# Optimization experiments

Measured on AMD Instinct MI355X. Metric: run time of the kernel, lower is better.

Reference implementation:

```python
import jax, jax.numpy as jnp
import numpy as np

B, S, E = 2, 2048, 1024
HID = 1024
HEADS = 16
EPS = 1e-5
SCALE = (E * 2) ** (-0.5)  # source uses input_data_dim*2


def setup_inputs() -> dict:
    key = jax.random.key(0)
    k1, k2, k3 = jax.random.split(key, 3)
    return {
        "x": jax.random.normal(k1, (B, S, E), dtype=jnp.float32),
        "ln_g": jnp.ones((E,), jnp.float32),
        "ln_b": jnp.zeros((E,), jnp.float32),
        "W1": jax.random.normal(k2, (E, 3 * HID), jnp.float32) * 0.02,
        "b1": jnp.zeros((3 * HID,), jnp.float32),
        "W2": jax.random.normal(k3, (HID, HID), jnp.float32) * 0.02,
        "b2": jnp.zeros((HID,), jnp.float32),
    }


def reference(x, ln_g, ln_b, W1, b1, W2, b2):
    # LayerNorm over last dim
    mu = jnp.mean(x, axis=-1, keepdims=True)
    var = jnp.mean(jnp.square(x - mu), axis=-1, keepdims=True)
    xn = (x - mu) * jax.lax.rsqrt(var + EPS) * ln_g + ln_b
    # QKV projection: [B,S,3*HID]
    qkv = jnp.einsum('bse,ef->bsf', xn, W1) + b1
    # Faithful to source: flat reshape to (heads, B, S, 3*HID/heads)
    qkv_heads = qkv.reshape(HEADS, B, S, -1)
    q, k, v = jnp.split(qkv_heads, 3, axis=-1)  # each [H,B,S,d]
    scores = jnp.einsum('hbse,hbSe->hbsS', q, k) * SCALE  # [H,B,S,S]
    att = jax.nn.softmax(scores, axis=-1)
    full_att = jnp.einsum('hbsS,hbSe->hbse', att, v)  # [H,B,S,d]
    full_att = full_att.reshape(B, S, -1)  # faithful flat reshape -> [B,S,HID]
    out = jnp.einsum('bsh,hk->bsk', full_att, W2) + b2
    return out
```

## Files before the change

### kernel.cpp

```cpp
#include <hip/hip_runtime.h>

typedef unsigned short u16;
typedef __bf16 bf16x8 __attribute__((ext_vector_type(8)));
typedef float f32x4 __attribute__((ext_vector_type(4)));

static constexpr float SCALE2 = 0.022097086912079608f * 1.4426950408889634f;

__device__ __forceinline__ u16 f2b(float f) {
  union { float f; unsigned int i; } v; v.f = f;
  unsigned int r = v.i + 0x7fffu + ((v.i >> 16) & 1u);
  return (u16)(r >> 16);
}
__device__ __forceinline__ unsigned int pk2(float a, float b) {
#if __has_builtin(__builtin_amdgcn_cvt_pk_bf16_f32)
  auto v = __builtin_amdgcn_cvt_pk_bf16_f32(a, b);
  unsigned int u;
  __builtin_memcpy(&u, &v, 4);
  return u;
#else
  union { float f; unsigned int i; } x, y; x.f = a; y.f = b;
  return ((x.i + 0x8000u) >> 16) | ((y.i + 0x8000u) & 0xffff0000u);
#endif
}
__device__ __forceinline__ void async16(const u16* g, u16* l) {
  __builtin_amdgcn_global_load_lds((const __attribute__((address_space(1))) void*)g,
                                   (__attribute__((address_space(3))) void*)l,
                                   16, 0, 0);
}

__global__ __launch_bounds__(256) void pre_kernel(const float* __restrict__ x,
                                                  const float* __restrict__ lg,
                                                  const float* __restrict__ lb,
                                                  u16* __restrict__ xn,
                                                  const float* __restrict__ W1,
                                                  u16* __restrict__ W1T,
                                                  const float* __restrict__ W2,
                                                  u16* __restrict__ W2T) {
  __shared__ __align__(16) u16 smem[64 * 72];
  const int bx = blockIdx.x;
  const int t = threadIdx.x;
  if (bx < 4096) {
    float* red = (float*)smem;
    const int row = bx;
    float4 v = *(const float4*)(x + (size_t)row * 1024 + t * 4);
    float s = v.x + v.y + v.z + v.w;
    float ss = v.x * v.x + v.y * v.y + v.z * v.z + v.w * v.w;
    for (int off = 32; off >= 1; off >>= 1) {
      s += __shfl_xor(s, off, 64);
      ss += __shfl_xor(ss, off, 64);
    }
    const int w = t >> 6;
    if ((t & 63) == 0) { red[w] = s; red[4 + w] = ss; }
    __syncthreads();
    s = red[0] + red[1] + red[2] + red[3];
    ss = red[4] + red[5] + red[6] + red[7];
    const float mu = s * (1.0f / 1024.0f);
    const float var = ss * (1.0f / 1024.0f) - mu * mu;
    const float inv = rsqrtf(var + 1e-5f);
    float4 gg = *(const float4*)(lg + t * 4);
    float4 bb = *(const float4*)(lb + t * 4);
    ushort4 o;
    o.x = f2b((v.x - mu) * inv * gg.x + bb.x);
    o.y = f2b((v.y - mu) * inv * gg.y + bb.y);
    o.z = f2b((v.z - mu) * inv * gg.z + bb.z);
    o.w = f2b((v.w - mu) * inv * gg.w + bb.w);
    *(ushort4*)(xn + (size_t)row * 1024 + t * 4) = o;
    return;
  }
  const float* in;
  u16* out;
  int C, c0, r0;
  if (bx < 4096 + 768) {
    const int idx = bx - 4096;
    C = 3072; in = W1; out = W1T;
    c0 = (idx % 48) * 64; r0 = (idx / 48) * 64;
  } else {
    const int idx = bx - 4864;
    C = 1024; in = W2; out = W2T;
    c0 = (idx % 16) * 64; r0 = (idx / 16) * 64;
  }
  const int row = t >> 2, cseg = t & 3;
  for (int it = 0; it < 4; it++) {
    float4 v = *(const float4*)&in[(size_t)(r0 + row) * C + c0 + it * 16 + cseg * 4];
    ushort4 o;
    o.x = f2b(v.x); o.y = f2b(v.y); o.z = f2b(v.z); o.w = f2b(v.w);
    *(ushort4*)&smem[row * 72 + it * 16 + cseg * 4] = o;
  }
  __syncthreads();
  const int orow = t >> 2, ch = t & 3;
  u16 vals[16];
  for (int j = 0; j < 16; j++) vals[j] = smem[(ch * 16 + j) * 72 + orow];
  u16* dp = out + (size_t)(c0 + orow) * 1024 + r0 + ch * 16;
  *(uint4*)&dp[0] = *(uint4*)&vals[0];
  *(uint4*)&dp[8] = *(uint4*)&vals[8];
}

template <int MODE, int MT>
__global__ __launch_bounds__(256) void gemm_bt(const u16* __restrict__ A,
                                               const u16* __restrict__ Bt,
                                               const float* __restrict__ bias,
                                               float* __restrict__ C,
                                               int M, int N, int K,
                                               u16* __restrict__ Qc,
                                               u16* __restrict__ Kc,
                                               u16* __restrict__ Vtmp) {
  __shared__ __align__(16) u16 SMEM[8192];
  u16* As = SMEM;
  u16* Bs = SMEM + MT * 32;
  const int m0 = blockIdx.y * MT, n0 = blockIdx.x * 128;
  const int t = threadIdx.x, w = t >> 6, lane = t & 63;
  const int q = lane >> 4, l16 = lane & 15;
  const int wm = (w >> 1) * (MT / 2), wn = (w & 1) * 64;
  constexpr int NI = MT / 32;

  const int sc = (lane & 3) ^ ((lane >> 3) & 3);
  const u16* ap = A + (size_t)(m0 + w * 16 + (lane >> 2)) * K + sc * 8;
  const u16* bp = Bt + (size_t)(n0 + w * 16 + (lane >> 2)) * K + sc * 8;
  u16* lA = &As[w * 512];
  u16* lB = &Bs[w * 512];
  const int ac = q ^ ((l16 >> 1) & 3);

  f32x4 acc[NI][4];
  const f32x4 zero = {0.f, 0.f, 0.f, 0.f};
  for (int i = 0; i < NI; i++)
    for (int j = 0; j < 4; j++) acc[i][j] = zero;

  for (int k0 = 0; k0 < K; k0 += 32) {
    for (int i = 0; i < MT / 64; i++)
      async16(ap + (size_t)(i * 64) * K, lA + i * 2048);
    for (int i = 0; i < 2; i++)
      async16(bp + (size_t)(i * 64) * K, lB + i * 2048);
    ap += 32; bp += 32;
    __syncthreads();
    bf16x8 af[NI], bfr[4];
    for (int i = 0; i < NI; i++)
      af[i] = *(const bf16x8*)&As[(wm + i * 16 + l16) * 32 + ac * 8];
    for (int j = 0; j < 4; j++)
      bfr[j] = *(const bf16x8*)&Bs[(wn + j * 16 + l16) * 32 + ac * 8];
    for (int i = 0; i < NI; i++)
      for (int j = 0; j < 4; j++)
        acc[i][j] = __builtin_amdgcn_mfma_f32_16x16x32_bf16(af[i], bfr[j], acc[i][j], 0, 0, 0);
    __syncthreads();
  }

  if constexpr (MODE == 0) {
    for (int j = 0; j < 4; j++) {
      const int col = n0 + wn + j * 16 + l16;
      const float bv = bias[col];
      for (int i = 0; i < NI; i++) {
        const int rbase = m0 + wm + i * 16 + q * 4;
        for (int r = 0; r < 4; r++)
          C[(size_t)(rbase + r) * N + col] = acc[i][j][r] + bv;
      }
    }
  } else {
    const int seg = n0 + wn;
    const int k64 = seg >> 6;
    const int tcol = k64 / 3;
    const int typ = k64 - tcol * 3;
    u16* dst = (typ == 0) ? Qc : (typ == 1) ? Kc : Vtmp;
    const float qs = (typ == 0) ? SCALE2 : 1.0f;
    const int gidx = m0 >> 7;
    u16* tw = &SMEM[w * 1280];
    float bv[4];
    for (int j = 0; j < 4; j++) bv[j] = bias[seg + j * 16 + l16];
    __syncthreads();
    for (int i = 0; i < 4; i++) {
      for (int j = 0; j < 4; j++) {
        ushort4 pk;
        pk.x = f2b((acc[i][j][0] + bv[j]) * qs);
        pk.y = f2b((acc[i][j][1] + bv[j]) * qs);
        pk.z = f2b((acc[i][j][2] + bv[j]) * qs);
        pk.w = f2b((acc[i][j][3] + bv[j]) * qs);
        *(ushort4*)&tw[(j * 16 + l16) * 20 + q * 4] = pk;
      }
      const int r2 = lane >> 2;
      const int quarter = lane & 3;
      u16 vals[16];
      for (int c = 0; c < 16; c++)
        vals[c] = tw[(quarter * 16 + c) * 20 + r2];
      const int lr = wm + i * 16 + r2;
      const int s = (lr << 4) + tcol;
      u16* dp = dst + ((size_t)gidx * 2048 + s) * 64 + quarter * 16;
      *(uint4*)&dp[0] = *(uint4*)&vals[0];
      *(uint4*)&dp[8] = *(uint4*)&vals[8];
    }
  }
}

__global__ __launch_bounds__(256) void vtrans(const u16* __restrict__ Vtmp,
                                              u16* __restrict__ Vt) {
  __shared__ __align__(16) u16 tile[64 * 64];
  const int g = blockIdx.y, s0 = blockIdx.x * 64;
  const int t = threadIdx.x;
  const int row = t >> 3, ch = t & 7;
  for (int p = 0; p < 2; p++) {
    const int r = p * 32 + row;
    uint4 v = *(const uint4*)&Vtmp[((size_t)g * 2048 + s0 + r) * 64 + ch * 8];
    *(uint4*)&tile[r * 64 + ((ch ^ (r & 7)) * 8)] = v;
  }
  __syncthreads();
  const int d = t >> 2, scn = t & 3;
  u16 vals[16];
  for (int j2 = 0; j2 < 16; j2++) {
    const int s = scn * 16 + j2;
    vals[j2] = tile[s * 64 + (((d >> 3) ^ (s & 7)) * 8) + (d & 7)];
  }
  u16* dp = Vt + ((size_t)g * 64 + d) * 2048 + s0 + scn * 16;
  *(uint4*)&dp[0] = *(uint4*)&vals[0];
  *(uint4*)&dp[8] = *(uint4*)&vals[8];
}

__global__ __launch_bounds__(256) void attn_kernel(const u16* __restrict__ Qc,
                                                   const u16* __restrict__ Kc,
                                                   const u16* __restrict__ Vt,
                                                   u16* __restrict__ Oc) {
  __shared__ __align__(16) u16 LDS[25600];
  u16* Ks = LDS;
  u16* Vs = LDS + 8192;
  u16* Ps = LDS + 16384;
  const int g = blockIdx.y;
  const int q0 = blockIdx.x * 128;
  const int t = threadIdx.x, w = t >> 6, lane = t & 63;
  const int q = lane >> 4, l16 = lane & 15;

  const u16* Qg = Qc + (size_t)g * 2048 * 64;
  const u16* Kg = Kc + (size_t)g * 2048 * 64;
  const u16* Vg = Vt + (size_t)g * 64 * 2048;

  bf16x8 aq[2][2];
  for (int rt = 0; rt < 2; rt++)
    for (int ks = 0; ks < 2; ks++)
      aq[rt][ks] = *(const bf16x8*)&Qg[(size_t)(q0 + w * 32 + rt * 16 + l16) * 64 + ks * 32 + q * 8];

  f32x4 accO[2][4];
  const f32x4 zero = {0.f, 0.f, 0.f, 0.f};
  for (int rt = 0; rt < 2; rt++)
    for (int c = 0; c < 4; c++) accO[rt][c] = zero;
  f32x4 psv[2] = {zero, zero};

  const int kc = (lane & 7) ^ ((lane >> 3) & 7);
  const int vc = (lane & 15) ^ ((w * 4 + (lane >> 4)) & 7);
  const u16* kp = Kg + (size_t)(w * 8 + (lane >> 3)) * 64 + kc * 8;
  const u16* vp = Vg + (size_t)(w * 4 + (lane >> 4)) * 2048 + vc * 8;
  u16* lK = &Ks[w * 512];
  u16* lV = &Vs[w * 512];

  const int kch = q ^ (l16 & 7);
  const int pb = w * 2304;

  for (int it = 0; it < 16; it++) {
    const int kt0 = it * 128;
    for (int i = 0; i < 4; i++) {
      async16(kp + (size_t)kt0 * 64 + i * 2048, lK + i * 2048);
      async16(vp + kt0 + (size_t)i * 32768, lV + i * 2048);
    }
    __syncthreads();

    f32x4 sa[2][8];
    for (int ct = 0; ct < 8; ct++) {
      bf16x8 bk0 = *(const bf16x8*)&Ks[(ct * 16 + l16) * 64 + kch * 8];
      bf16x8 bk1 = *(const bf16x8*)&Ks[(ct * 16 + l16) * 64 + (kch ^ 4) * 8];
      for (int rt = 0; rt < 2; rt++) {
        f32x4 a = zero;
        a = __builtin_amdgcn_mfma_f32_16x16x32_bf16(bk0, aq[rt][0], a, 0, 0, 0);
        a = __builtin_amdgcn_mfma_f32_16x16x32_bf16(bk1, aq[rt][1], a, 0, 0, 0);
        sa[rt][ct] = a;
      }
    }

    for (int ph = 0; ph < 2; ph++) {
      for (int rt = 0; rt < 2; rt++) {
        u16* Pr = &Ps[pb + rt * 1152 + l16 * 72];
        for (int c4 = 0; c4 < 4; c4++) {
          const int ct = ph * 4 + c4;
          f32x4 p;
          for (int r = 0; r < 4; r++) p[r] = __builtin_amdgcn_exp2f(sa[rt][ct][r]);
          psv[rt] += p;
          uint2 pk;
          pk.x = pk2(p[0], p[1]);
          pk.y = pk2(p[2], p[3]);
          *(uint2*)&Pr[c4 * 16 + q * 4] = pk;
        }
      }
      for (int k2 = 0; k2 < 2; k2++) {
        const int ks2 = ph * 2 + k2;
        bf16x8 apf[2];
        for (int rt = 0; rt < 2; rt++)
          apf[rt] = *(const bf16x8*)&Ps[pb + rt * 1152 + l16 * 72 + k2 * 32 + q * 8];
        for (int c = 0; c < 4; c++) {
          const int vch = (ks2 * 4 + q) ^ (l16 & 7);
          bf16x8 bv = *(const bf16x8*)&Vs[(c * 16 + l16) * 128 + vch * 8];
          for (int rt = 0; rt < 2; rt++)
            accO[rt][c] = __builtin_amdgcn_mfma_f32_16x16x32_bf16(bv, apf[rt], accO[rt][c], 0, 0, 0);
        }
      }
    }
    __syncthreads();
  }

  for (int rt = 0; rt < 2; rt++) {
    float lsum = psv[rt][0] + psv[rt][1] + psv[rt][2] + psv[rt][3];
    lsum += __shfl_xor(lsum, 16, 64);
    lsum += __shfl_xor(lsum, 32, 64);
    const int srow = q0 + w * 32 + rt * 16 + l16;
    const int orow = g * 128 + (srow >> 4);
    const int cbase = (srow & 15) * 64;
    const float linv = 1.0f / lsum;
    for (int c = 0; c < 4; c++) {
      ushort4 o;
      o.x = f2b(accO[rt][c][0] * linv);
      o.y = f2b(accO[rt][c][1] * linv);
      o.z = f2b(accO[rt][c][2] * linv);
      o.w = f2b(accO[rt][c][3] * linv);
      *(ushort4*)&Oc[(size_t)orow * 1024 + cbase + c * 16 + q * 4] = o;
    }
  }
}

extern "C" void kernel_launch(void* const* d_in, const int* in_sizes, int n_in,
                              void* d_out, int out_size, void* d_ws, size_t ws_size,
                              hipStream_t stream) {
  (void)in_sizes; (void)n_in; (void)out_size; (void)ws_size;
  const float* x    = (const float*)d_in[0];
  const float* ln_g = (const float*)d_in[1];
  const float* ln_b = (const float*)d_in[2];
  const float* W1   = (const float*)d_in[3];
  const float* b1   = (const float*)d_in[4];
  const float* W2   = (const float*)d_in[5];
  const float* b2   = (const float*)d_in[6];

  char* ws = (char*)d_ws;
  u16* xn   = (u16*)(ws);
  u16* W1T  = (u16*)(ws + ((size_t)8 << 20));
  u16* W2T  = (u16*)(ws + ((size_t)14 << 20));
  u16* Qc   = (u16*)(ws + ((size_t)16 << 20));
  u16* Kc   = (u16*)(ws + ((size_t)24 << 20));
  u16* Vtmp = (u16*)(ws + ((size_t)32 << 20));
  u16* Vt   = (u16*)(ws + ((size_t)40 << 20));
  u16* Oc   = xn;

  pre_kernel<<<dim3(5120), dim3(256), 0, stream>>>(x, ln_g, ln_b, xn, W1, W1T, W2, W2T);
  gemm_bt<1, 128><<<dim3(24, 32), dim3(256), 0, stream>>>(xn, W1T, b1, nullptr,
                                                          4096, 3072, 1024, Qc, Kc, Vtmp);
  vtrans<<<dim3(32, 32), dim3(256), 0, stream>>>(Vtmp, Vt);
  attn_kernel<<<dim3(16, 32), dim3(256), 0, stream>>>(Qc, Kc, Vt, Oc);
  gemm_bt<0, 64><<<dim3(8, 64), dim3(256), 0, stream>>>(Oc, W2T, b2, (float*)d_out,
                                                        4096, 1024, 1024, nullptr, nullptr, nullptr);
}
```

Measured before the change: 204.6 us.

## Double-buffer K/V tiles in attention kernel with async prefetch of next tile

Splits the key/value tile from 128 to 64 keys and uses two LDS buffers so the async loads for the next tile are issued before computing on the current one, overlapping global-to-LDS transfer with MFMA work. It also raises wave priority around the MFMA sections with s_setprio. The cost is twice as many iterations and barriers per block. The async load completion also appears to depend on the single end-of-iteration barrier.

```diff
diff --git a/kernel.cpp b/kernel.cpp
--- a/kernel.cpp
+++ b/kernel.cpp
@@ -216,8 +216,10 @@
                                                    const u16* __restrict__ Vt,
                                                    u16* __restrict__ Oc) {
   __shared__ __align__(16) u16 LDS[25600];
-  u16* Ks = LDS;
-  u16* Vs = LDS + 8192;
+  u16* K0 = LDS;
+  u16* K1 = LDS + 4096;
+  u16* V0 = LDS + 8192;
+  u16* V1 = LDS + 12288;
   u16* Ps = LDS + 16384;
   const int g = blockIdx.y;
   const int q0 = blockIdx.x * 128;
@@ -239,28 +241,42 @@
     for (int c = 0; c < 4; c++) accO[rt][c] = zero;
   f32x4 psv[2] = {zero, zero};
 
-  const int kc = (lane & 7) ^ ((lane >> 3) & 7);
-  const int vc = (lane & 15) ^ ((w * 4 + (lane >> 4)) & 7);
-  const u16* kp = Kg + (size_t)(w * 8 + (lane >> 3)) * 64 + kc * 8;
-  const u16* vp = Vg + (size_t)(w * 4 + (lane >> 4)) * 2048 + vc * 8;
-  u16* lK = &Ks[w * 512];
-  u16* lV = &Vs[w * 512];
+  const int ch = (lane & 7) ^ ((lane >> 3) & 7);
+  const u16* kp = Kg + (size_t)(w * 8 + (lane >> 3)) * 64 + ch * 8;
+  const u16* vp = Vg + (size_t)(w * 8 + (lane >> 3)) * 2048 + ch * 8;
+  u16* lK0 = K0 + w * 512;
+  u16* lK1 = K1 + w * 512;
+  u16* lV0 = V0 + w * 512;
+  u16* lV1 = V1 + w * 512;
 
   const int kch = q ^ (l16 & 7);
   const int pb = w * 2304;
 
-  for (int it = 0; it < 16; it++) {
-    const int kt0 = it * 128;
-    for (int i = 0; i < 4; i++) {
-      async16(kp + (size_t)kt0 * 64 + i * 2048, lK + i * 2048);
-      async16(vp + kt0 + (size_t)i * 32768, lV + i * 2048);
-    }
-    __syncthreads();
-
-    f32x4 sa[2][8];
-    for (int ct = 0; ct < 8; ct++) {
-      bf16x8 bk0 = *(const bf16x8*)&Ks[(ct * 16 + l16) * 64 + kch * 8];
-      bf16x8 bk1 = *(const bf16x8*)&Ks[(ct * 16 + l16) * 64 + (kch ^ 4) * 8];
+  for (int i = 0; i < 2; i++) {
+    async16(kp + i * 2048, lK0 + i * 2048);
+    async16(vp + (size_t)i * 65536, lV0 + i * 2048);
+  }
+  __syncthreads();
+
+  for (int it = 0; it < 32; it++) {
+    const int cur = it & 1;
+    const u16* Kcur = cur ? K1 : K0;
+    const u16* Vcur = cur ? V1 : V0;
+    if (it < 31) {
+      u16* Kn = cur ? lK0 : lK1;
+      u16* Vn = cur ? lV0 : lV1;
+      const int kt0 = (it + 1) * 64;
+      for (int i = 0; i < 2; i++) {
+        async16(kp + (size_t)kt0 * 64 + i * 2048, Kn + i * 2048);
+        async16(vp + kt0 + (size_t)i * 65536, Vn + i * 2048);
+      }
+    }
+
+    f32x4 sa[2][4];
+    __builtin_amdgcn_s_setprio(1);
+    for (int ct = 0; ct < 4; ct++) {
+      bf16x8 bk0 = *(const bf16x8*)&Kcur[(ct * 16 + l16) * 64 + kch * 8];
+      bf16x8 bk1 = *(const bf16x8*)&Kcur[(ct * 16 + l16) * 64 + (kch ^ 4) * 8];
       for (int rt = 0; rt < 2; rt++) {
         f32x4 a = zero;
         a = __builtin_amdgcn_mfma_f32_16x16x32_bf16(bk0, aq[rt][0], a, 0, 0, 0);
@@ -268,34 +284,35 @@
         sa[rt][ct] = a;
       }
     }
-
-    for (int ph = 0; ph < 2; ph++) {
-      for (int rt = 0; rt < 2; rt++) {
-        u16* Pr = &Ps[pb + rt * 1152 + l16 * 72];
-        for (int c4 = 0; c4 < 4; c4++) {
-          const int ct = ph * 4 + c4;
-          f32x4 p;
-          for (int r = 0; r < 4; r++) p[r] = __builtin_amdgcn_exp2f(sa[rt][ct][r]);
-          psv[rt] += p;
-          uint2 pk;
-          pk.x = pk2(p[0], p[1]);
-          pk.y = pk2(p[2], p[3]);
-          *(uint2*)&Pr[c4 * 16 + q * 4] = pk;
-        }
-      }
-      for (int k2 = 0; k2 < 2; k2++) {
-        const int ks2 = ph * 2 + k2;
-        bf16x8 apf[2];
+    __builtin_amdgcn_s_setprio(0);
+
+    for (int rt = 0; rt < 2; rt++) {
+      u16* Pr = &Ps[pb + rt * 1152 + l16 * 72];
+      for (int ct = 0; ct < 4; ct++) {
+        f32x4 p;
+        for (int r = 0; r < 4; r++) p[r] = __builtin_amdgcn_exp2f(sa[rt][ct][r]);
+        psv[rt] += p;
+        uint2 pk;
+        pk.x = pk2(p[0], p[1]);
+        pk.y = pk2(p[2], p[3]);
+        *(uint2*)&Pr[ct * 16 + q * 4] = pk;
+      }
+    }
+
+    __builtin_amdgcn_s_setprio(1);
+    for (int k2 = 0; k2 < 2; k2++) {
+      bf16x8 apf[2];
+      for (int rt = 0; rt < 2; rt++)
+        apf[rt] = *(const bf16x8*)&Ps[pb + rt * 1152 + l16 * 72 + k2 * 32 + q * 8];
+      for (int c = 0; c < 4; c++) {
+        const int vch = (k2 * 4 + q) ^ (l16 & 7);
+        bf16x8 bv = *(const bf16x8*)&Vcur[(c * 16 + l16) * 64 + vch * 8];
         for (int rt = 0; rt < 2; rt++)
-          apf[rt] = *(const bf16x8*)&Ps[pb + rt * 1152 + l16 * 72 + k2 * 32 + q * 8];
-        for (int c = 0; c < 4; c++) {
-          const int vch = (ks2 * 4 + q) ^ (l16 & 7);
-          bf16x8 bv = *(const bf16x8*)&Vs[(c * 16 + l16) * 128 + vch * 8];
-          for (int rt = 0; rt < 2; rt++)
-            accO[rt][c] = __builtin_amdgcn_mfma_f32_16x16x32_bf16(bv, apf[rt], accO[rt][c], 0, 0, 0);
-        }
-      }
-    }
+          accO[rt][c] = __builtin_amdgcn_mfma_f32_16x16x32_bf16(bv, apf[rt], accO[rt][c], 0, 0, 0);
+      }
+    }
+    __builtin_amdgcn_s_setprio(0);
+
     __syncthreads();
   }
 
```

Measured after the change: 205.9 us. About the same (+0.6%).
